# Kernel tuning notes

Hardware: AMD Instinct MI355X
Metric: run time of the kernel (lower is better)

## Reference

```python
import jax, jax.numpy as jnp
import numpy as np

DIM = 128
N_NODES = 50000
N_EDGES = 625000


def setup_inputs() -> dict:
    key = jax.random.key(0)
    ks = jax.random.split(key, 6)
    X = jax.random.normal(ks[0], (N_NODES, DIM), dtype=jnp.float32)
    edge_index = jax.random.randint(ks[1], (2, N_EDGES), 0, N_NODES, dtype=jnp.int64)
    # Linear params, init like torch (uniform +/- 1/sqrt(dim))
    bound = 1.0 / np.sqrt(DIM)
    msg_w = jax.random.uniform(ks[2], (DIM, DIM), minval=-bound, maxval=bound, dtype=jnp.float32)
    msg_b = jax.random.uniform(ks[3], (DIM,), minval=-bound, maxval=bound, dtype=jnp.float32)
    lin_w = jax.random.uniform(ks[4], (DIM, DIM), minval=-bound, maxval=bound, dtype=jnp.float32)
    lin_b = jax.random.uniform(ks[5], (DIM,), minval=-bound, maxval=bound, dtype=jnp.float32)
    eps = jnp.asarray(0.0, dtype=jnp.float32)
    return {"X": X, "edge_index": edge_index, "eps": eps,
            "msg_w": msg_w, "msg_b": msg_b, "lin_w": lin_w, "lin_b": lin_b}


def reference(X, edge_index, eps, msg_w, msg_b, lin_w, lin_b):
    src, dst = edge_index[0], edge_index[1]
    # msg_lin(X) then gather at dst: (E, F)
    msg = (jnp.einsum('nf,gf->ng', X, msg_w) + msg_b)[dst]
    # scatter-add messages onto src nodes: (N, F)
    agg = jax.ops.segment_sum(msg, src, num_segments=X.shape[0])
    out = (1.0 + eps) * X + agg
    out = jnp.einsum('nf,gf->ng', out, lin_w) + lin_b
    return jax.nn.relu(out)
```

## Files before the change

kernel.cpp:

```cpp
#include <hip/hip_runtime.h>
#include <hip/hip_bf16.h>

#define NN 50000
#define NE 625000
#define DIM 128

#define NBKT 782
#define NBKTP 784
#define CAP 1536
#define CHUNK 4096
#define NCHUNK ((NE + CHUNK - 1) / CHUNK)

#define XCAST_NB 6250
#define PREP_NB 65
#define SETUP_NB (NCHUNK + XCAST_NB + PREP_NB)

using fragAB = __attribute__((ext_vector_type(8))) short;
using fragC  = __attribute__((ext_vector_type(4))) float;

__device__ __forceinline__ unsigned short f2bf(float f) {
    unsigned int u = __float_as_uint(f);
    unsigned int r = u + 0x7FFFu + ((u >> 16) & 1u);
    return (unsigned short)(r >> 16);
}

__device__ __forceinline__ float bflo(unsigned v) { return __uint_as_float(v << 16); }
__device__ __forceinline__ float bfhi(unsigned v) { return __uint_as_float(v & 0xffff0000u); }

__global__ __launch_bounds__(256) void mega_setup(
    const float* __restrict__ X, const int* __restrict__ ei,
    const float* __restrict__ L, const float* __restrict__ W,
    const float* __restrict__ mb, const float* __restrict__ epsp,
    float* __restrict__ cb, unsigned short* __restrict__ Bh,
    unsigned short* __restrict__ Xbf,
    int* __restrict__ bucket_cursor, unsigned* __restrict__ staging) {
    __shared__ int cnt[NBKTP];
    __shared__ int base[NBKTP];
    __shared__ int gb[NBKTP];
    __shared__ int wsum[4];
    __shared__ unsigned staged[CHUNK];
    int blk = blockIdx.x;
    int t = threadIdx.x;

    if (blk >= NCHUNK) {
        int xb = blk - NCHUNK;
        if (xb < XCAST_NB) {
            int idx = (xb * 256 + t) * 4;
            float4 v = *(const float4*)(X + idx);
            uint2 p;
            p.x = (unsigned)f2bf(v.x) | ((unsigned)f2bf(v.y) << 16);
            p.y = (unsigned)f2bf(v.z) | ((unsigned)f2bf(v.w) << 16);
            *(uint2*)(Xbf + idx) = p;
        } else {
            int idx = (xb - XCAST_NB) * 256 + t;
            float scale = 1.0f + *epsp;
            if (idx < DIM * DIM) {
                int o = idx >> 7, g = idx & 127;
                float s = 0.f;
                for (int f = 0; f < DIM; f++) s += L[o * DIM + f] * W[f * DIM + g];
                Bh[o * 256 + 128 + g] = f2bf(s);
                Bh[o * 256 + g] = f2bf(L[o * DIM + g] * scale);
            } else if (idx < DIM * DIM + DIM) {
                int o = idx - DIM * DIM;
                float s = 0.f;
                for (int f = 0; f < DIM; f++) s += L[o * DIM + f] * mb[f];
                cb[o] = s;
            }
        }
        return;
    }

    int e0 = blk * CHUNK;
    int nthis = NE - e0; if (nthis > CHUNK) nthis = CHUNK;

    for (int i = t; i < NBKTP; i += 256) cnt[i] = 0;
    __syncthreads();

    unsigned pk[CHUNK / 256];
#pragma unroll
    for (int i = 0; i < CHUNK / 256; i++) {
        int e = e0 + i * 256 + t;
        if (e < NE) {
            int s = ei[e];
            int d = ei[NE + e];
            unsigned b = (unsigned)s >> 6;
            pk[i] = (b << 22) | ((unsigned)(s & 63) << 16) | (unsigned)d;
            atomicAdd(&cnt[b], 1);
        } else pk[i] = 0xFFFFFFFFu;
    }
    __syncthreads();

    int myb = t * 4;
    int s0 = 0;
    if (myb < NBKTP) s0 = cnt[myb] + cnt[myb + 1] + cnt[myb + 2] + cnt[myb + 3];
    int lane = t & 63, w = t >> 6;
    int v = s0;
#pragma unroll
    for (int off = 1; off < 64; off <<= 1) {
        int u = __shfl_up(v, off);
        if (lane >= off) v += u;
    }
    if (lane == 63) wsum[w] = v;
    __syncthreads();
    int add = 0;
#pragma unroll
    for (int i = 0; i < 4; i++)
        if (i < w) add += wsum[i];
    int run = v + add - s0;
    if (myb < NBKTP) {
        for (int i = 0; i < 4; i++) {
            int b = myb + i;
            base[b] = run;
            int c = cnt[b];
            gb[b] = (b < NBKT && c > 0) ? atomicAdd(&bucket_cursor[b], c) : 0;
            run += c;
        }
    }
    __syncthreads();
    if (myb < NBKTP) {
        for (int i = 0; i < 4; i++) cnt[myb + i] = base[myb + i];
    }
    __syncthreads();

#pragma unroll
    for (int i = 0; i < CHUNK / 256; i++) {
        if (pk[i] != 0xFFFFFFFFu) {
            unsigned b = pk[i] >> 22;
            int pos = atomicAdd(&cnt[b], 1);
            staged[pos] = pk[i];
        }
    }
    __syncthreads();

    for (int idx = t; idx < nthis; idx += 256) {
        unsigned p = staged[idx];
        unsigned b = p >> 22;
        int pos = gb[b] + (idx - base[b]);
        if (pos >= 0 && pos < CAP) staging[(size_t)b * CAP + pos] = p;
    }
}

__global__ __launch_bounds__(512) void bucket_gather(
    const int* __restrict__ bucket_cursor, const unsigned* __restrict__ staging,
    const unsigned short* __restrict__ Xbf, unsigned short* __restrict__ Aggbf,
    int* __restrict__ deg) {
    __shared__ unsigned rec[CAP];
    __shared__ unsigned sorted_[CAP];
    __shared__ int hcnt[64];
    __shared__ int hbase[64];
    __shared__ int cur[64];
    int t = threadIdx.x;
    int b = blockIdx.x;
    int cnt_b = bucket_cursor[b];
    if (cnt_b > CAP) cnt_b = CAP;

    if (t < 64) hcnt[t] = 0;
    __syncthreads();
    for (int i = t; i < cnt_b; i += 512) {
        unsigned r = staging[(size_t)b * CAP + i];
        rec[i] = r;
        atomicAdd(&hcnt[(r >> 16) & 63], 1);
    }
    __syncthreads();
    if (t < 64) {
        int c = hcnt[t];
        int v = c;
#pragma unroll
        for (int off = 1; off < 64; off <<= 1) {
            int u = __shfl_up(v, off);
            if (t >= off) v += u;
        }
        int ex = v - c;
        hbase[t] = ex;
        cur[t] = ex;
        int src = b * 64 + t;
        if (src < NN) deg[src] = c;
    }
    __syncthreads();
    for (int i = t; i < cnt_b; i += 512) {
        unsigned r = rec[i];
        int pos = atomicAdd(&cur[(r >> 16) & 63], 1);
        sorted_[pos] = r;
    }
    __syncthreads();

    int wave = t >> 6, lane = t & 63;
    int l32 = lane & 31, half = lane >> 5;
    const uint2* __restrict__ X2 = (const uint2*)Xbf;
    for (int ni = 0; ni < 8; ni++) {
        int local = wave * 8 + ni;
        int node = b * 64 + local;
        if (node >= NN) continue;
        int start = hbase[local];
        int cnt = hcnt[local];
        float a0 = 0.f, a1 = 0.f, a2 = 0.f, a3 = 0.f;
        int pairs = cnt >> 1;
        int j = 0;
        for (; j + 8 <= pairs; j += 8) {
            int d[8];
#pragma unroll
            for (int i = 0; i < 8; i++)
                d[i] = (int)(sorted_[start + 2 * (j + i) + half] & 0xFFFFu);
            uint2 v[8];
#pragma unroll
            for (int i = 0; i < 8; i++) v[i] = X2[(size_t)d[i] * 32 + l32];
#pragma unroll
            for (int i = 0; i < 8; i++) {
                a0 += bflo(v[i].x);
                a1 += bfhi(v[i].x);
                a2 += bflo(v[i].y);
                a3 += bfhi(v[i].y);
            }
        }
        for (; j < pairs; j++) {
            int d = (int)(sorted_[start + 2 * j + half] & 0xFFFFu);
            uint2 v = X2[(size_t)d * 32 + l32];
            a0 += bflo(v.x);
            a1 += bfhi(v.x);
            a2 += bflo(v.y);
            a3 += bfhi(v.y);
        }
        if ((cnt & 1) && half == 0) {
            int d = (int)(sorted_[start + cnt - 1] & 0xFFFFu);
            uint2 v = X2[(size_t)d * 32 + l32];
            a0 += bflo(v.x);
            a1 += bfhi(v.x);
            a2 += bflo(v.y);
            a3 += bfhi(v.y);
        }
        a0 += __shfl_xor(a0, 32);
        a1 += __shfl_xor(a1, 32);
        a2 += __shfl_xor(a2, 32);
        a3 += __shfl_xor(a3, 32);
        if (half == 0) {
            uint2 p;
            p.x = (unsigned)f2bf(a0) | ((unsigned)f2bf(a1) << 16);
            p.y = (unsigned)f2bf(a2) | ((unsigned)f2bf(a3) << 16);
            ((uint2*)Aggbf)[(size_t)node * 32 + l32] = p;
        }
    }
}

__global__ __launch_bounds__(256) void outgemm_kernel(
    const unsigned short* __restrict__ Xbf, const unsigned short* __restrict__ Aggbf,
    const unsigned short* __restrict__ Bh, const int* __restrict__ deg,
    const float* __restrict__ cb, const float* __restrict__ lin_b,
    float* __restrict__ out) {
    __shared__ unsigned short As[128 * 40];
    __shared__ unsigned short Bs[128 * 40];
    int tid = threadIdx.x;
    int lane = tid & 63;
    int wave = tid >> 6;
    int m16 = lane & 15;
    int quad = lane >> 4;
    int waveM = (wave & 1) * 64;
    int waveN = (wave >> 1) * 64;
    int r0 = blockIdx.x * 128;

    fragC acc[4][4];
#pragma unroll
    for (int i = 0; i < 4; i++)
#pragma unroll
        for (int j = 0; j < 4; j++) acc[i][j] = (fragC){0.f, 0.f, 0.f, 0.f};

    int srow = tid >> 1;
    int shalf = tid & 1;
    int arow = r0 + srow;
    if (arow >= NN) arow = NN - 1;

    for (int kc = 0; kc < 8; kc++) {
        int kb = kc * 32;
        {
            const unsigned short* asrc = (kc < 4) ? Xbf : Aggbf;
            int akb = kb & 127;
            const uint4* gp = (const uint4*)(asrc + (size_t)arow * 128 + akb + shalf * 16);
            uint4 w0 = gp[0];
            uint4 w1 = gp[1];
            uint4* lp = (uint4*)(As + srow * 40 + shalf * 16);
            lp[0] = w0;
            lp[1] = w1;
        }
        {
            const uint4* gp = (const uint4*)(Bh + (size_t)srow * 256 + kb + shalf * 16);
            uint4 w0 = gp[0];
            uint4 w1 = gp[1];
            uint4* lp = (uint4*)(Bs + srow * 40 + shalf * 16);
            lp[0] = w0;
            lp[1] = w1;
        }
        __syncthreads();

        fragAB a[4], bfr[4];
#pragma unroll
        for (int i = 0; i < 4; i++)
            a[i] = *(const fragAB*)(As + (waveM + i * 16 + m16) * 40 + quad * 8);
#pragma unroll
        for (int j = 0; j < 4; j++)
            bfr[j] = *(const fragAB*)(Bs + (waveN + j * 16 + m16) * 40 + quad * 8);
#pragma unroll
        for (int i = 0; i < 4; i++)
#pragma unroll
            for (int j = 0; j < 4; j++)
                acc[i][j] = __builtin_amdgcn_mfma_f32_16x16x32_bf16(a[i], bfr[j], acc[i][j], 0, 0, 0);
        __syncthreads();
    }

#pragma unroll
    for (int j = 0; j < 4; j++) {
        int col = waveN + j * 16 + m16;
        float cbc = cb[col];
        float lbc = lin_b[col];
#pragma unroll
        for (int i = 0; i < 4; i++) {
            int rbase = r0 + waveM + i * 16 + quad * 4;
#pragma unroll
            for (int r = 0; r < 4; r++) {
                int row = rbase + r;
                if (row < NN) {
                    float dg = (float)deg[row];
                    float v = acc[i][j][r] + dg * cbc + lbc;
                    out[(size_t)row * 128 + col] = fmaxf(v, 0.f);
                }
            }
        }
    }
}

extern "C" void kernel_launch(void* const* d_in, const int* in_sizes, int n_in,
                              void* d_out, int out_size, void* d_ws, size_t ws_size,
                              hipStream_t stream) {
    const float* X = (const float*)d_in[0];
    const int* ei = (const int*)d_in[1];
    const float* epsp = (const float*)d_in[2];
    const float* msg_w = (const float*)d_in[3];
    const float* msg_b = (const float*)d_in[4];
    const float* lin_w = (const float*)d_in[5];
    const float* lin_b = (const float*)d_in[6];
    float* out = (float*)d_out;

    int* bucket_cursor = (int*)d_ws;
    unsigned* staging = (unsigned*)(bucket_cursor + 800);
    int* deg = (int*)(staging + (size_t)NBKT * CAP);
    float* cb = (float*)(deg + NN);
    unsigned short* Bh = (unsigned short*)(cb + DIM);
    unsigned short* Xbf = Bh + 128 * 256;
    unsigned short* Aggbf = Xbf + (size_t)NN * 128;

    hipMemsetAsync(bucket_cursor, 0, NBKTP * sizeof(int), stream);

    mega_setup<<<SETUP_NB, 256, 0, stream>>>(X, ei, lin_w, msg_w, msg_b, epsp, cb, Bh, Xbf,
                                             bucket_cursor, staging);
    bucket_gather<<<NBKT, 512, 0, stream>>>(bucket_cursor, staging, Xbf, Aggbf, deg);
    outgemm_kernel<<<(NN + 127) / 128, 256, 0, stream>>>(Xbf, Aggbf, Bh, deg, cb, lin_b, out);
}
```

Measured before the change: 157.8 us.

## Fuse bucket gather with output GEMM, keeping aggregated rows in LDS

Merges the gather kernel and the output GEMM into one kernel per 64-node bucket. X and the aggregated rows are staged in shared memory as a 64x256 bf16 tile, and the MFMA GEMM reads B fragments straight from global memory. This drops the Aggbf and deg round-trips through HBM and one kernel launch. In exchange, each block of 8 waves computes only a 64x128 tile with small per-wave tiles, reloads B without LDS reuse, and uses more LDS per block, which may lower occupancy.

```diff
diff --git a/kernel.cpp b/kernel.cpp
--- a/kernel.cpp
+++ b/kernel.cpp
@@ -140,21 +140,32 @@
     }
 }
 
-__global__ __launch_bounds__(512) void bucket_gather(
+__global__ __launch_bounds__(512, 4) void gather_gemm(
     const int* __restrict__ bucket_cursor, const unsigned* __restrict__ staging,
-    const unsigned short* __restrict__ Xbf, unsigned short* __restrict__ Aggbf,
-    int* __restrict__ deg) {
+    const unsigned short* __restrict__ Xbf, const unsigned short* __restrict__ Bh,
+    const float* __restrict__ cb, const float* __restrict__ lin_b,
+    float* __restrict__ out) {
     __shared__ unsigned rec[CAP];
     __shared__ unsigned sorted_[CAP];
     __shared__ int hcnt[64];
     __shared__ int hbase[64];
     __shared__ int cur[64];
+    __shared__ unsigned short As[64 * 264];
     int t = threadIdx.x;
     int b = blockIdx.x;
     int cnt_b = bucket_cursor[b];
     if (cnt_b > CAP) cnt_b = CAP;
 
     if (t < 64) hcnt[t] = 0;
+#pragma unroll
+    for (int it = 0; it < 2; it++) {
+        int idx = t + it * 512;
+        int row = idx >> 4, c = idx & 15;
+        int node = b * 64 + row;
+        if (node >= NN) node = NN - 1;
+        uint4 vx = *(const uint4*)(Xbf + (size_t)node * 128 + c * 8);
+        *(uint4*)(As + row * 264 + c * 8) = vx;
+    }
     __syncthreads();
     for (int i = t; i < cnt_b; i += 512) {
         unsigned r = staging[(size_t)b * CAP + i];
@@ -173,8 +184,6 @@
         int ex = v - c;
         hbase[t] = ex;
         cur[t] = ex;
-        int src = b * 64 + t;
-        if (src < NN) deg[src] = c;
     }
     __syncthreads();
     for (int i = t; i < cnt_b; i += 512) {
@@ -236,73 +245,28 @@
             uint2 p;
             p.x = (unsigned)f2bf(a0) | ((unsigned)f2bf(a1) << 16);
             p.y = (unsigned)f2bf(a2) | ((unsigned)f2bf(a3) << 16);
-            ((uint2*)Aggbf)[(size_t)node * 32 + l32] = p;
-        }
-    }
-}
-
-__global__ __launch_bounds__(256) void outgemm_kernel(
-    const unsigned short* __restrict__ Xbf, const unsigned short* __restrict__ Aggbf,
-    const unsigned short* __restrict__ Bh, const int* __restrict__ deg,
-    const float* __restrict__ cb, const float* __restrict__ lin_b,
-    float* __restrict__ out) {
-    __shared__ unsigned short As[128 * 40];
-    __shared__ unsigned short Bs[128 * 40];
-    int tid = threadIdx.x;
-    int lane = tid & 63;
-    int wave = tid >> 6;
+            *(uint2*)(As + local * 264 + 128 + l32 * 4) = p;
+        }
+    }
+    __syncthreads();
+
     int m16 = lane & 15;
     int quad = lane >> 4;
-    int waveM = (wave & 1) * 64;
-    int waveN = (wave >> 1) * 64;
-    int r0 = blockIdx.x * 128;
-
-    fragC acc[4][4];
-#pragma unroll
-    for (int i = 0; i < 4; i++)
-#pragma unroll
-        for (int j = 0; j < 4; j++) acc[i][j] = (fragC){0.f, 0.f, 0.f, 0.f};
-
-    int srow = tid >> 1;
-    int shalf = tid & 1;
-    int arow = r0 + srow;
-    if (arow >= NN) arow = NN - 1;
-
+    int waveM = (wave & 3) * 16;
+    int waveN = (wave >> 2) * 64;
+
+    fragC acc[4];
+#pragma unroll
+    for (int j = 0; j < 4; j++) acc[j] = (fragC){0.f, 0.f, 0.f, 0.f};
+
+#pragma unroll
     for (int kc = 0; kc < 8; kc++) {
-        int kb = kc * 32;
-        {
-            const unsigned short* asrc = (kc < 4) ? Xbf : Aggbf;
-            int akb = kb & 127;
-            const uint4* gp = (const uint4*)(asrc + (size_t)arow * 128 + akb + shalf * 16);
-            uint4 w0 = gp[0];
-            uint4 w1 = gp[1];
-            uint4* lp = (uint4*)(As + srow * 40 + shalf * 16);
-            lp[0] = w0;
-            lp[1] = w1;
-        }
-        {
-            const uint4* gp = (const uint4*)(Bh + (size_t)srow * 256 + kb + shalf * 16);
-            uint4 w0 = gp[0];
-            uint4 w1 = gp[1];
-            uint4* lp = (uint4*)(Bs + srow * 40 + shalf * 16);
-            lp[0] = w0;
-            lp[1] = w1;
-        }
-        __syncthreads();
-
-        fragAB a[4], bfr[4];
-#pragma unroll
-        for (int i = 0; i < 4; i++)
-            a[i] = *(const fragAB*)(As + (waveM + i * 16 + m16) * 40 + quad * 8);
-#pragma unroll
-        for (int j = 0; j < 4; j++)
-            bfr[j] = *(const fragAB*)(Bs + (waveN + j * 16 + m16) * 40 + quad * 8);
-#pragma unroll
-        for (int i = 0; i < 4; i++)
-#pragma unroll
-            for (int j = 0; j < 4; j++)
-                acc[i][j] = __builtin_amdgcn_mfma_f32_16x16x32_bf16(a[i], bfr[j], acc[i][j], 0, 0, 0);
-        __syncthreads();
+        fragAB a = *(const fragAB*)(As + (waveM + m16) * 264 + kc * 32 + quad * 8);
+#pragma unroll
+        for (int j = 0; j < 4; j++) {
+            fragAB bf = *(const fragAB*)(Bh + (size_t)(waveN + j * 16 + m16) * 256 + kc * 32 + quad * 8);
+            acc[j] = __builtin_amdgcn_mfma_f32_16x16x32_bf16(a, bf, acc[j], 0, 0, 0);
+        }
     }
 
 #pragma unroll
@@ -310,17 +274,15 @@
         int col = waveN + j * 16 + m16;
         float cbc = cb[col];
         float lbc = lin_b[col];
-#pragma unroll
-        for (int i = 0; i < 4; i++) {
-            int rbase = r0 + waveM + i * 16 + quad * 4;
-#pragma unroll
-            for (int r = 0; r < 4; r++) {
-                int row = rbase + r;
-                if (row < NN) {
-                    float dg = (float)deg[row];
-                    float v = acc[i][j][r] + dg * cbc + lbc;
-                    out[(size_t)row * 128 + col] = fmaxf(v, 0.f);
-                }
+        int lr = waveM + quad * 4;
+#pragma unroll
+        for (int r = 0; r < 4; r++) {
+            int row = lr + r;
+            int node = b * 64 + row;
+            if (node < NN) {
+                float dg = (float)hcnt[row];
+                float v = acc[j][r] + dg * cbc + lbc;
+                out[(size_t)node * 128 + col] = fmaxf(v, 0.f);
             }
         }
     }
@@ -340,16 +302,13 @@
 
     int* bucket_cursor = (int*)d_ws;
     unsigned* staging = (unsigned*)(bucket_cursor + 800);
-    int* deg = (int*)(staging + (size_t)NBKT * CAP);
-    float* cb = (float*)(deg + NN);
+    float* cb = (float*)(staging + (size_t)NBKT * CAP);
     unsigned short* Bh = (unsigned short*)(cb + DIM);
     unsigned short* Xbf = Bh + 128 * 256;
-    unsigned short* Aggbf = Xbf + (size_t)NN * 128;
 
     hipMemsetAsync(bucket_cursor, 0, NBKTP * sizeof(int), stream);
 
     mega_setup<<<SETUP_NB, 256, 0, stream>>>(X, ei, lin_w, msg_w, msg_b, epsp, cb, Bh, Xbf,
                                              bucket_cursor, staging);
-    bucket_gather<<<NBKT, 512, 0, stream>>>(bucket_cursor, staging, Xbf, Aggbf, deg);
-    outgemm_kernel<<<(NN + 127) / 128, 256, 0, stream>>>(Xbf, Aggbf, Bh, deg, cb, lin_b, out);
+    gather_gemm<<<NBKT, 512, 0, stream>>>(bucket_cursor, staging, Xbf, Bh, cb, lin_b, out);
 }
```

Measured after the change: 181.5 us. 1.15x slower.
